# Kernel optimization log

Measured on AMD Instinct MI355X. Metric: run time of the kernel, lower is better.

The kernel has to match this reference:

```python
import jax, jax.numpy as jnp
import numpy as np

B, T, E = 2, 2048, 2048
H, D = 16, 128          # n_head, head_dim = E // H
RQ, RK, RV = 6, 2, 2    # TPA ranks


def setup_inputs() -> dict:
    key = jax.random.key(0)
    ks = jax.random.split(key, 8)
    x = jax.random.normal(ks[0], (B, T, E), jnp.float32)
    # RoPE tables: cos/sin of shape (T, 1, D//2) broadcast over (B,T,R,D//2)
    half = D // 2
    inv_freq = 1.0 / (10000.0 ** (jnp.arange(half, dtype=jnp.float32) / half))
    ang = jnp.arange(T, dtype=jnp.float32)[:, None] * inv_freq[None, :]
    cos = jnp.cos(ang)[:, None, :]
    sin = jnp.sin(ang)[:, None, :]
    s = 0.02
    W_aQ = (jax.random.normal(ks[1], (RQ * H, E), jnp.float32) * s)
    W_bQ = (jax.random.normal(ks[2], (RQ * D, E), jnp.float32) * s)
    W_aK = (jax.random.normal(ks[3], (RK * H, E), jnp.float32) * s)
    W_bK = (jax.random.normal(ks[4], (RK * D, E), jnp.float32) * s)
    W_aV = (jax.random.normal(ks[5], (RV * H, E), jnp.float32) * s)
    W_bV = (jax.random.normal(ks[6], (RV * D, E), jnp.float32) * s)
    W_cproj = (jax.random.normal(ks[7], (E, E), jnp.float32) * s)
    return {"x": x, "cos": cos, "sin": sin, "W_aQ": W_aQ, "W_bQ": W_bQ,
            "W_aK": W_aK, "W_bK": W_bK, "W_aV": W_aV, "W_bV": W_bV,
            "W_cproj": W_cproj}


def _rope(xb, cos, sin):
    # xb: (B, T, R, D); rotate-half style on split halves of D
    d = xb.shape[-1] // 2
    x1, x2 = xb[..., :d], xb[..., d:]
    return jnp.concatenate([x1 * cos + x2 * sin, -x1 * sin + x2 * cos], axis=-1)


def _rmsnorm(x):
    # F.rms_norm with no weight, default eps = finfo(dtype).eps
    eps = jnp.finfo(x.dtype).eps
    return x * jax.lax.rsqrt(jnp.mean(x * x, axis=-1, keepdims=True) + eps)


def reference(x, cos, sin, W_aQ, W_bQ, W_aK, W_bK, W_aV, W_bV, W_cproj):
    # low-rank factor projections
    a_q = (x @ W_aQ.T).reshape(B, T, RQ, H)
    a_k = (x @ W_aK.T).reshape(B, T, RK, H)
    a_v = (x @ W_aV.T).reshape(B, T, RV, H)
    b_q = (x @ W_bQ.T).reshape(B, T, RQ, D)
    b_k = (x @ W_bK.T).reshape(B, T, RK, D)
    b_v = (x @ W_bV.T).reshape(B, T, RV, D)
    # RoPE on the b factors (equivalent to RoPE on materialized Q/K)
    b_q = _rope(b_q, cos, sin)
    b_k = _rope(b_k, cos, sin)
    # tensor-product contraction: (B,T,H,D)
    q = jnp.einsum('btrh,btrd->bthd', a_q, b_q) / RQ
    k = jnp.einsum('btrh,btrd->bthd', a_k, b_k) / RK
    v = jnp.einsum('btrh,btrd->bthd', a_v, b_v) / RV
    q = _rmsnorm(q)
    k = _rmsnorm(k)
    # causal SDPA (kv_cache=None, window_size=None)
    scale = 1.0 / jnp.sqrt(jnp.asarray(D, q.dtype))
    scores = jnp.einsum('bthd,bshd->bhts', q, k) * scale
    causal = jnp.tril(jnp.ones((T, T), dtype=bool))
    scores = jnp.where(causal, scores, jnp.asarray(-jnp.inf, scores.dtype))
    p = jax.nn.softmax(scores, axis=-1)
    y = jnp.einsum('bhts,bshd->bthd', p, v).reshape(B, T, E)
    return y @ W_cproj.T
```

## Files before the change

kernel.cpp:

```cpp
#include <hip/hip_runtime.h>
#include <stdint.h>

typedef unsigned short ushort_t;
typedef __attribute__((ext_vector_type(8))) short s16x8;
typedef __attribute__((ext_vector_type(4))) float f32x4;
typedef __attribute__((ext_vector_type(16))) float f32x16;
typedef __attribute__((ext_vector_type(4))) unsigned int u32x4;

__device__ __forceinline__ unsigned short f2bf(float x) {
  union { float f; unsigned u; } a; a.f = x;
  unsigned r = a.u + 0x7fffu + ((a.u >> 16) & 1u);
  return (unsigned short)(r >> 16);
}
__device__ __forceinline__ float bf2f(unsigned short u) {
  union { unsigned u; float f; } a; a.u = ((unsigned)u) << 16;
  return a.f;
}
__device__ __forceinline__ unsigned cvtpk(float lo, float hi) {
  unsigned r;
  asm("v_cvt_pk_bf16_f32 %0, %1, %2" : "=v"(r) : "v"(lo), "v"(hi));
  return r;
}
__device__ __forceinline__ void gll16(const ushort_t* g, ushort_t* l) {
  __builtin_amdgcn_global_load_lds((const __attribute__((address_space(1))) void*)g,
                                   (__attribute__((address_space(3))) void*)l, 16, 0, 0);
}

__global__ void cvt4(const float* __restrict__ s, ushort_t* __restrict__ d, int n4) {
  int idx = blockIdx.x * blockDim.x + threadIdx.x;
  if (idx >= n4) return;
  const float4 v = *(const float4*)(s + (size_t)idx * 4);
  ushort4 o;
  o.x = f2bf(v.x); o.y = f2bf(v.y); o.z = f2bf(v.z); o.w = f2bf(v.w);
  *(ushort4*)(d + (size_t)idx * 4) = o;
}

__global__ void build_wcat(const float* __restrict__ aQ, const float* __restrict__ aK,
                           const float* __restrict__ aV, const float* __restrict__ bQ,
                           const float* __restrict__ bK, const float* __restrict__ bV,
                           ushort_t* __restrict__ W) {
  int idx = blockIdx.x * blockDim.x + threadIdx.x;
  if (idx >= 1536 * 2048) return;
  int row = idx >> 11, col = idx & 2047;
  float v = 0.f;
  if (row < 96)        v = aQ[row * 2048 + col];
  else if (row < 128)  v = aK[(row - 96) * 2048 + col];
  else if (row < 160)  v = aV[(row - 128) * 2048 + col];
  else if (row < 928)  v = bQ[(row - 160) * 2048 + col];
  else if (row < 1184) v = bK[(row - 928) * 2048 + col];
  else if (row < 1440) v = bV[(row - 1184) * 2048 + col];
  W[idx] = f2bf(v);
}

__global__ __launch_bounds__(256, 2) void gemm_bt(
    const ushort_t* __restrict__ A, const ushort_t* __restrict__ B,
    float* __restrict__ C, int M, int N, int K, int NT) {
  __shared__ ushort_t Asm[2][128 * 64];
  __shared__ ushort_t Bsm[2][128 * 64];
  const int bid = blockIdx.x;
  const int mt = bid / NT, nt = bid % NT;
  const int tid = threadIdx.x;
  const int lane = tid & 63;
  const int w = tid >> 6, wr = w >> 1, wc = w & 1;
  const int wbase = (tid & ~63);

  f32x4 acc[4][4];
#pragma unroll
  for (int a1 = 0; a1 < 4; ++a1)
#pragma unroll
    for (int b1 = 0; b1 < 4; ++b1)
#pragma unroll
      for (int e = 0; e < 4; ++e) acc[a1][b1][e] = 0.f;

  const int nkt = K >> 6;

  auto STAGE = [&](int buf, int kt) {
#pragma unroll
    for (int i = 0; i < 4; ++i) {
      int g = i * 256 + tid;
      int row = g >> 3, sc = g & 7;
      int scc = sc ^ (row & 7);
      gll16(A + (size_t)(mt * 128 + row) * K + kt * 64 + scc * 8,
            &Asm[buf][(i * 256 + wbase) * 8]);
      gll16(B + (size_t)(nt * 128 + row) * K + kt * 64 + scc * 8,
            &Bsm[buf][(i * 256 + wbase) * 8]);
    }
  };

  STAGE(0, 0);
  asm volatile("s_waitcnt vmcnt(0)" ::: "memory");
  __syncthreads();
  int cur = 0;
  for (int kt = 0; kt < nkt; ++kt) {
    if (kt + 1 < nkt) STAGE(cur ^ 1, kt + 1);
#pragma unroll
    for (int ks = 0; ks < 2; ++ks) {
      s16x8 af[4], bfv[4];
#pragma unroll
      for (int mi = 0; mi < 4; ++mi) {
        int row = wr * 64 + mi * 16 + (lane & 15);
        int colc = ks * 4 + (lane >> 4);
        af[mi] = *(const s16x8*)&Asm[cur][(row * 8 + (colc ^ (row & 7))) * 8];
      }
#pragma unroll
      for (int ni = 0; ni < 4; ++ni) {
        int row = wc * 64 + ni * 16 + (lane & 15);
        int colc = ks * 4 + (lane >> 4);
        bfv[ni] = *(const s16x8*)&Bsm[cur][(row * 8 + (colc ^ (row & 7))) * 8];
      }
#pragma unroll
      for (int mi = 0; mi < 4; ++mi)
#pragma unroll
        for (int ni = 0; ni < 4; ++ni)
          acc[mi][ni] = __builtin_amdgcn_mfma_f32_16x16x32_bf16(af[mi], bfv[ni], acc[mi][ni], 0, 0, 0);
    }
    asm volatile("s_waitcnt vmcnt(0)" ::: "memory");
    __syncthreads();
    cur ^= 1;
  }
#pragma unroll
  for (int mi = 0; mi < 4; ++mi) {
    int row0 = mt * 128 + wr * 64 + mi * 16 + ((lane >> 4) << 2);
#pragma unroll
    for (int ni = 0; ni < 4; ++ni) {
      int col = nt * 128 + wc * 64 + ni * 16 + (lane & 15);
#pragma unroll
      for (int e = 0; e < 4; ++e)
        C[(size_t)(row0 + e) * N + col] = acc[mi][ni][e];
    }
  }
}

__global__ __launch_bounds__(256) void fuse_qkv(
    const float* __restrict__ Cp, const float* __restrict__ cosT, const float* __restrict__ sinT,
    ushort_t* __restrict__ qb, ushort_t* __restrict__ kb, ushort_t* __restrict__ vb) {
  const int tok = blockIdx.x;
  const int b = tok >> 11, t = tok & 2047;
  const float* __restrict__ row = Cp + (size_t)tok * 1536;
  __shared__ float aq[96], ak[32], av[32];
  __shared__ float rbq[768], rbk[256], bvs[256];
  __shared__ float cs[64], sn[64];
  const int tid = threadIdx.x;
  if (tid < 96)        aq[tid] = row[tid];
  else if (tid < 128)  ak[tid - 96] = row[tid];
  else if (tid < 160)  av[tid - 128] = row[tid];
  else if (tid < 224) { cs[tid - 160] = cosT[t * 64 + tid - 160];
                        sn[tid - 160] = sinT[t * 64 + tid - 160]; }
  __syncthreads();
  for (int p = tid; p < 384; p += 256) {
    int r = p >> 6, d = p & 63;
    float x1 = row[160 + r * 128 + d], x2 = row[160 + r * 128 + 64 + d];
    rbq[r * 128 + d]      = x1 * cs[d] + x2 * sn[d];
    rbq[r * 128 + 64 + d] = x2 * cs[d] - x1 * sn[d];
  }
  if (tid < 128) {
    int r = tid >> 6, d = tid & 63;
    float x1 = row[928 + r * 128 + d], x2 = row[928 + r * 128 + 64 + d];
    rbk[r * 128 + d]      = x1 * cs[d] + x2 * sn[d];
    rbk[r * 128 + 64 + d] = x2 * cs[d] - x1 * sn[d];
  } else {
    int p = tid - 128;
    bvs[p] = row[1184 + p];
    bvs[p + 128] = row[1184 + 128 + p];
  }
  __syncthreads();
  const int w = tid >> 6, lane = tid & 63;
  const float QSC = 0.12751744154127828f;
#pragma unroll
  for (int j = 0; j < 4; ++j) {
    int h = w + 4 * j;
    float q0 = 0.f, q1 = 0.f;
#pragma unroll
    for (int r = 0; r < 6; ++r) {
      float a = aq[r * 16 + h];
      q0 += a * rbq[r * 128 + lane];
      q1 += a * rbq[r * 128 + 64 + lane];
    }
    q0 *= (1.f / 6.f); q1 *= (1.f / 6.f);
    float ss = q0 * q0 + q1 * q1;
#pragma unroll
    for (int o = 32; o; o >>= 1) ss += __shfl_xor(ss, o);
    float rms = rsqrtf(ss * (1.f / 128.f) + 1.1920929e-7f) * QSC;
    size_t base = ((size_t)(b * 16 + h) * 2048 + t) * 128;
    qb[base + lane]      = f2bf(q0 * rms);
    qb[base + 64 + lane] = f2bf(q1 * rms);
  }
#pragma unroll
  for (int j = 0; j < 4; ++j) {
    int h = w + 4 * j;
    float k0 = ak[h] * rbk[lane]      + ak[16 + h] * rbk[128 + lane];
    float k1 = ak[h] * rbk[64 + lane] + ak[16 + h] * rbk[192 + lane];
    k0 *= 0.5f; k1 *= 0.5f;
    float ss = k0 * k0 + k1 * k1;
#pragma unroll
    for (int o = 32; o; o >>= 1) ss += __shfl_xor(ss, o);
    float rms = rsqrtf(ss * (1.f / 128.f) + 1.1920929e-7f);
    size_t base = ((size_t)(b * 16 + h) * 2048 + t) * 128;
    kb[base + lane]      = f2bf(k0 * rms);
    kb[base + 64 + lane] = f2bf(k1 * rms);
    float v0 = 0.5f * (av[h] * bvs[lane]      + av[16 + h] * bvs[128 + lane]);
    float v1 = 0.5f * (av[h] * bvs[64 + lane] + av[16 + h] * bvs[192 + lane]);
    vb[base + lane]      = f2bf(v0);
    vb[base + 64 + lane] = f2bf(v1);
  }
}

__global__ __launch_bounds__(256) void transpose_v(const ushort_t* __restrict__ src,
                                                   ushort_t* __restrict__ dst) {
  __shared__ ushort_t sm[64 * 128];
  const int tt = blockIdx.x, bh = blockIdx.y;
  const size_t base = (size_t)bh * (2048 * 128);
  const int tid = threadIdx.x;
#pragma unroll
  for (int it = 0; it < 4; ++it) {
    int c = it * 256 + tid;
    int t = c >> 4, dc = c & 15;
    u32x4 v = *(const u32x4*)(src + base + (size_t)(tt * 64 + t) * 128 + dc * 8);
    *(u32x4*)&sm[(t * 16 + (dc ^ (t & 15))) * 8] = v;
  }
  __syncthreads();
#pragma unroll
  for (int it = 0; it < 4; ++it) {
    int c = it * 256 + tid;
    int d = c >> 3, tc = c & 7;
    ushort_t tmp[8];
#pragma unroll
    for (int jj = 0; jj < 8; ++jj) {
      int t = tc * 8 + jj;
      tmp[jj] = sm[(t * 16 + ((d >> 3) ^ (t & 15))) * 8 + (d & 7)];
    }
    *(u32x4*)(dst + base + (size_t)d * 2048 + tt * 64 + tc * 8) = *(const u32x4*)tmp;
  }
}

__global__ __launch_bounds__(256, 2) void attn(
    const ushort_t* __restrict__ Q, const ushort_t* __restrict__ Kt,
    const ushort_t* __restrict__ VT, ushort_t* __restrict__ Y,
    ushort_t* __restrict__ Ppart, float* __restrict__ Spart) {
  static const short JQT[24]  = {8,9,10,11,12,13,14,15,15,7,14,6,13,5,12,4,11,3,10,2,9,1,8,0};
  static const short JKLO[24] = {0,0,0,0,0,0,0,0,8,0,8,0,8,0,8,0,8,0,8,0,8,0,8,0};
  static const short JKHI[24] = {8,8,8,8,8,8,8,8,16,8,15,7,14,6,13,5,12,4,11,3,10,2,9,1};
  static const short JMODE[24]= {1,1,1,1,1,1,1,1,2,0,2,0,2,0,2,0,2,0,2,0,2,0,2,0};
  __shared__ ushort_t Ksm[2][64 * 128];
  __shared__ ushort_t Vsm[2][128 * 64];
  const int j = blockIdx.y, bh = blockIdx.x;
  const int qt = JQT[j];
  const int klo = (int)JKLO[j] * 128;
  const int mode = JMODE[j];
  const int kend_blk_raw = (int)JKHI[j] * 128;
  const int kend_blk = (kend_blk_raw < qt * 128 + 128) ? kend_blk_raw : qt * 128 + 128;
  const int b = bh >> 4, h = bh & 15;
  const int tid = threadIdx.x, lane = tid & 63, w = tid >> 6;
  const int hi = lane >> 5, li = lane & 31;
  const int wbase = (tid & ~63);
  const size_t hbase = (size_t)bh * (2048 * 128);
  const int wq0 = qt * 128 + w * 32;
  const int i = wq0 + li;

  s16x8 qf[8];
  const ushort_t* qrow = Q + hbase + (size_t)i * 128 + hi * 8;
#pragma unroll
  for (int c = 0; c < 8; ++c) qf[c] = *(const s16x8*)(qrow + c * 16);

  f32x16 o[4];
#pragma unroll
  for (int dt = 0; dt < 4; ++dt)
#pragma unroll
    for (int e = 0; e < 16; ++e) o[dt][e] = 0.f;
  float ssum = 0.f;

  auto STAGE = [&](int buf, int kv0s) {
#pragma unroll
    for (int it = 0; it < 4; ++it) {
      int g = it * 256 + tid;
      int row = g >> 4, sc = g & 15;
      gll16(Kt + hbase + (size_t)(kv0s + row) * 128 + (sc ^ (row & 7)) * 8,
            &Ksm[buf][(it * 256 + wbase) * 8]);
    }
#pragma unroll
    for (int it = 0; it < 4; ++it) {
      int g = it * 256 + tid;
      int d = g >> 3, sc = g & 7;
      gll16(VT + hbase + (size_t)d * 2048 + kv0s + (sc ^ (d & 7)) * 8,
            &Vsm[buf][(it * 256 + wbase) * 8]);
    }
  };

  const int nt = (kend_blk - klo) >> 6;
  STAGE(0, klo);
  asm volatile("s_waitcnt vmcnt(0)" ::: "memory");
  __syncthreads();
  int cur = 0;
  for (int t = 0; t < nt; ++t) {
    const int kv0 = klo + t * 64;
    if (t + 1 < nt) STAGE(cur ^ 1, kv0 + 64);
#pragma unroll
    for (int s = 0; s < 2; ++s) {
      const int kvs = kv0 + s * 32;
      if (kvs < wq0 + 32) {
        const int krow = s * 32 + li;
        s16x8 kf[8];
#pragma unroll
        for (int c = 0; c < 8; ++c)
          kf[c] = *(const s16x8*)&Ksm[cur][(krow * 16 + ((2 * c + hi) ^ (krow & 7))) * 8];
        f32x16 st;
#pragma unroll
        for (int e = 0; e < 16; ++e) st[e] = 0.f;
        __builtin_amdgcn_s_setprio(1);
#pragma unroll
        for (int c = 0; c < 8; ++c)
          st = __builtin_amdgcn_mfma_f32_32x32x16_bf16(kf[c], qf[c], st, 0, 0, 0);
        __builtin_amdgcn_s_setprio(0);
        float p[16]; float ls = 0.f;
        if (kvs == wq0) {
#pragma unroll
          for (int r = 0; r < 16; ++r) {
            int jrow = kvs + (r & 3) + 8 * (r >> 2) + 4 * hi;
            float pv = exp2f(st[r]);
            p[r] = (jrow > i) ? 0.f : pv;
            ls += p[r];
          }
        } else {
#pragma unroll
          for (int r = 0; r < 16; ++r) { p[r] = exp2f(st[r]); ls += p[r]; }
        }
        ls += __shfl_xor(ls, 32);
        ssum += ls;
        unsigned xp[8], xw[8];
#pragma unroll
        for (int q2 = 0; q2 < 8; ++q2) xp[q2] = cvtpk(p[2 * q2], p[2 * q2 + 1]);
#pragma unroll
        for (int q2 = 0; q2 < 8; ++q2) xw[q2] = (unsigned)__shfl_xor((int)xp[q2], 32);
        __builtin_amdgcn_s_setprio(1);
#pragma unroll
        for (int c2 = 0; c2 < 2; ++c2) {
          union { s16x8 v; unsigned u[4]; } pu;
          pu.u[0] = hi ? xw[4 * c2 + 2] : xp[4 * c2];
          pu.u[1] = hi ? xw[4 * c2 + 3] : xp[4 * c2 + 1];
          pu.u[2] = hi ? xp[4 * c2 + 2] : xw[4 * c2];
          pu.u[3] = hi ? xp[4 * c2 + 3] : xw[4 * c2 + 1];
#pragma unroll
          for (int dt = 0; dt < 4; ++dt) {
            int d = dt * 32 + li;
            s16x8 vf = *(const s16x8*)&Vsm[cur][(d * 8 + ((4 * s + 2 * c2 + hi) ^ (d & 7))) * 8];
            o[dt] = __builtin_amdgcn_mfma_f32_32x32x16_bf16(pu.v, vf, o[dt], 0, 0, 0);
          }
        }
        __builtin_amdgcn_s_setprio(0);
      }
    }
    asm volatile("s_waitcnt vmcnt(0)" ::: "memory");
    __syncthreads();
    cur ^= 1;
  }

  if (mode == 2) {
    ushort_t* Pb = Ppart + (size_t)(bh * 8 + qt - 8) * 16384;
    if (hi == 0) Spart[((size_t)bh * 16 + 8 + qt - 8) * 128 + w * 32 + li] = ssum;
#pragma unroll
    for (int r = 0; r < 16; ++r) {
      int rr = (r & 3) + 8 * (r >> 2) + 4 * hi;
#pragma unroll
      for (int dt = 0; dt < 4; ++dt)
        Pb[(size_t)(w * 32 + rr) * 128 + dt * 32 + li] = f2bf(o[dt][r]);
    }
  } else {
    if (mode == 1 && hi == 0)
      Spart[((size_t)bh * 16 + qt - 8) * 128 + w * 32 + li] = ssum;
#pragma unroll
    for (int r = 0; r < 16; ++r) {
      int rr = (r & 3) + 8 * (r >> 2) + 4 * hi;
      float rs = __shfl(ssum, rr);
      float inv = (mode == 0) ? 1.f / rs : 1.f;
      size_t yrow = (size_t)(b * 2048 + wq0 + rr);
#pragma unroll
      for (int dt = 0; dt < 4; ++dt)
        Y[yrow * 2048 + h * 128 + dt * 32 + li] = f2bf(o[dt][r] * inv);
    }
  }
}

__global__ __launch_bounds__(256) void combine(ushort_t* __restrict__ Y,
                                               const ushort_t* __restrict__ Ppart,
                                               const float* __restrict__ Spart) {
  const int qt = 8 + blockIdx.x, bh = blockIdx.y;
  const int b = bh >> 4, h = bh & 15;
  const ushort_t* Pb = Ppart + (size_t)(bh * 8 + qt - 8) * 16384;
  const float* s0 = Spart + ((size_t)bh * 16 + qt - 8) * 128;
  const float* s1 = s0 + 8 * 128;
#pragma unroll
  for (int it = 0; it < 8; ++it) {
    int c = it * 256 + threadIdx.x;
    int r = c >> 4, dc = c & 15;
    ushort_t* yp = Y + ((size_t)(b * 2048 + qt * 128 + r)) * 2048 + h * 128 + dc * 8;
    u32x4 o0 = *(const u32x4*)yp;
    u32x4 o1 = *(const u32x4*)(Pb + (size_t)r * 128 + dc * 8);
    float inv = 1.f / (s0[r] + s1[r]);
    const ushort_t* a = (const ushort_t*)&o0;
    const ushort_t* bq = (const ushort_t*)&o1;
    ushort_t res[8];
#pragma unroll
    for (int e = 0; e < 8; ++e) res[e] = f2bf((bf2f(a[e]) + bf2f(bq[e])) * inv);
    *(u32x4*)yp = *(const u32x4*)res;
  }
}

extern "C" void kernel_launch(void* const* d_in, const int* in_sizes, int n_in,
                              void* d_out, int out_size, void* d_ws, size_t ws_size,
                              hipStream_t stream) {
  const float* x    = (const float*)d_in[0];
  const float* cosT = (const float*)d_in[1];
  const float* sinT = (const float*)d_in[2];
  const float* W_aQ = (const float*)d_in[3];
  const float* W_bQ = (const float*)d_in[4];
  const float* W_aK = (const float*)d_in[5];
  const float* W_bK = (const float*)d_in[6];
  const float* W_aV = (const float*)d_in[7];
  const float* W_bV = (const float*)d_in[8];
  const float* W_c  = (const float*)d_in[9];
  float* out = (float*)d_out;

  char* ws = (char*)d_ws;
  ushort_t* xb    = (ushort_t*)(ws);
  ushort_t* Wcat  = (ushort_t*)(ws + 16777216);
  ushort_t* Wcb   = (ushort_t*)(ws + 23068672);
  float*    Cp    = (float*)   (ws + 31457280);
  ushort_t* qb    = (ushort_t*)(ws + 56623104);
  ushort_t* kb    = (ushort_t*)(ws + 73400320);
  ushort_t* vb    = (ushort_t*)(ws + 90177536);
  ushort_t* yb    = xb;
  ushort_t* vt    = (ushort_t*)(ws + 31457280);
  ushort_t* Ppart = (ushort_t*)(ws + 48234496);
  float*    Spart = (float*)   (ws + 16777216);

  cvt4<<<8192, 256, 0, stream>>>(x, xb, 2097152);
  build_wcat<<<12288, 256, 0, stream>>>(W_aQ, W_aK, W_aV, W_bQ, W_bK, W_bV, Wcat);
  cvt4<<<4096, 256, 0, stream>>>(W_c, Wcb, 1048576);

  gemm_bt<<<384, 256, 0, stream>>>(xb, Wcat, Cp, 4096, 1536, 2048, 12);
  fuse_qkv<<<4096, 256, 0, stream>>>(Cp, cosT, sinT, qb, kb, vb);
  transpose_v<<<dim3(32, 32), 256, 0, stream>>>(vb, vt);
  attn<<<dim3(32, 24), 256, 0, stream>>>(qb, kb, vt, yb, Ppart, Spart);
  combine<<<dim3(8, 32), 256, 0, stream>>>(yb, Ppart, Spart);
  gemm_bt<<<512, 256, 0, stream>>>(yb, Wcb, out, 4096, 2048, 2048, 16);
}
```

Before: 192.7 us.

## Rebalance causal attention work into 16 blocks per head with paired tasks

Reworks the attention grid from 24 to 16 blocks per head. Each block runs one or two query-tile tasks in sequence, pairing short causal tiles with split halves of long tiles so per-block work is more even. Split-K now applies only to query tiles 9-15, and the combine kernel and partial-buffer indexing are adjusted to match. It also swaps the cross-half lane exchange to permlane32_swap when that builtin is available, which cuts shuffle instructions. The cost is fewer blocks in flight and a serial second task per block.

```diff
diff --git a/kernel.cpp b/kernel.cpp
--- a/kernel.cpp
+++ b/kernel.cpp
@@ -237,37 +237,19 @@
     const ushort_t* __restrict__ Q, const ushort_t* __restrict__ Kt,
     const ushort_t* __restrict__ VT, ushort_t* __restrict__ Y,
     ushort_t* __restrict__ Ppart, float* __restrict__ Spart) {
-  static const short JQT[24]  = {8,9,10,11,12,13,14,15,15,7,14,6,13,5,12,4,11,3,10,2,9,1,8,0};
-  static const short JKLO[24] = {0,0,0,0,0,0,0,0,8,0,8,0,8,0,8,0,8,0,8,0,8,0,8,0};
-  static const short JKHI[24] = {8,8,8,8,8,8,8,8,16,8,15,7,14,6,13,5,12,4,11,3,10,2,9,1};
-  static const short JMODE[24]= {1,1,1,1,1,1,1,1,2,0,2,0,2,0,2,0,2,0,2,0,2,0,2,0};
+  static const signed char T1QT[16] = {15,15,14,14,13,13,12,12,11,11,10,10, 9, 9, 8, 7};
+  static const signed char T1LO[16] = { 0, 9, 0, 9, 0, 9, 0, 9, 0, 9, 0, 9, 0, 9, 0, 0};
+  static const signed char T1HI[16] = { 9,16, 9,15, 9,14, 9,13, 9,12, 9,11, 9,10, 9, 8};
+  static const signed char T1MD[16] = { 1, 2, 1, 2, 1, 2, 1, 2, 1, 2, 1, 2, 1, 2, 0, 0};
+  static const signed char T2QT[16] = {-1, 0,-1, 1,-1, 2,-1, 3,-1, 4,-1, 5,-1, 6,-1,-1};
   __shared__ ushort_t Ksm[2][64 * 128];
   __shared__ ushort_t Vsm[2][128 * 64];
   const int j = blockIdx.y, bh = blockIdx.x;
-  const int qt = JQT[j];
-  const int klo = (int)JKLO[j] * 128;
-  const int mode = JMODE[j];
-  const int kend_blk_raw = (int)JKHI[j] * 128;
-  const int kend_blk = (kend_blk_raw < qt * 128 + 128) ? kend_blk_raw : qt * 128 + 128;
   const int b = bh >> 4, h = bh & 15;
   const int tid = threadIdx.x, lane = tid & 63, w = tid >> 6;
   const int hi = lane >> 5, li = lane & 31;
   const int wbase = (tid & ~63);
   const size_t hbase = (size_t)bh * (2048 * 128);
-  const int wq0 = qt * 128 + w * 32;
-  const int i = wq0 + li;
-
-  s16x8 qf[8];
-  const ushort_t* qrow = Q + hbase + (size_t)i * 128 + hi * 8;
-#pragma unroll
-  for (int c = 0; c < 8; ++c) qf[c] = *(const s16x8*)(qrow + c * 16);
-
-  f32x16 o[4];
-#pragma unroll
-  for (int dt = 0; dt < 4; ++dt)
-#pragma unroll
-    for (int e = 0; e < 16; ++e) o[dt][e] = 0.f;
-  float ssum = 0.f;
 
   auto STAGE = [&](int buf, int kv0s) {
 #pragma unroll
@@ -286,96 +268,147 @@
     }
   };
 
-  const int nt = (kend_blk - klo) >> 6;
-  STAGE(0, klo);
-  asm volatile("s_waitcnt vmcnt(0)" ::: "memory");
-  __syncthreads();
-  int cur = 0;
-  for (int t = 0; t < nt; ++t) {
-    const int kv0 = klo + t * 64;
-    if (t + 1 < nt) STAGE(cur ^ 1, kv0 + 64);
-#pragma unroll
-    for (int s = 0; s < 2; ++s) {
-      const int kvs = kv0 + s * 32;
-      if (kvs < wq0 + 32) {
-        const int krow = s * 32 + li;
-        s16x8 kf[8];
-#pragma unroll
-        for (int c = 0; c < 8; ++c)
-          kf[c] = *(const s16x8*)&Ksm[cur][(krow * 16 + ((2 * c + hi) ^ (krow & 7))) * 8];
-        f32x16 st;
-#pragma unroll
-        for (int e = 0; e < 16; ++e) st[e] = 0.f;
-        __builtin_amdgcn_s_setprio(1);
-#pragma unroll
-        for (int c = 0; c < 8; ++c)
-          st = __builtin_amdgcn_mfma_f32_32x32x16_bf16(kf[c], qf[c], st, 0, 0, 0);
-        __builtin_amdgcn_s_setprio(0);
-        float p[16]; float ls = 0.f;
-        if (kvs == wq0) {
-#pragma unroll
-          for (int r = 0; r < 16; ++r) {
-            int jrow = kvs + (r & 3) + 8 * (r >> 2) + 4 * hi;
-            float pv = exp2f(st[r]);
-            p[r] = (jrow > i) ? 0.f : pv;
-            ls += p[r];
-          }
-        } else {
-#pragma unroll
-          for (int r = 0; r < 16; ++r) { p[r] = exp2f(st[r]); ls += p[r]; }
-        }
-        ls += __shfl_xor(ls, 32);
-        ssum += ls;
-        unsigned xp[8], xw[8];
-#pragma unroll
-        for (int q2 = 0; q2 < 8; ++q2) xp[q2] = cvtpk(p[2 * q2], p[2 * q2 + 1]);
-#pragma unroll
-        for (int q2 = 0; q2 < 8; ++q2) xw[q2] = (unsigned)__shfl_xor((int)xp[q2], 32);
-        __builtin_amdgcn_s_setprio(1);
-#pragma unroll
-        for (int c2 = 0; c2 < 2; ++c2) {
-          union { s16x8 v; unsigned u[4]; } pu;
-          pu.u[0] = hi ? xw[4 * c2 + 2] : xp[4 * c2];
-          pu.u[1] = hi ? xw[4 * c2 + 3] : xp[4 * c2 + 1];
-          pu.u[2] = hi ? xp[4 * c2 + 2] : xw[4 * c2];
-          pu.u[3] = hi ? xp[4 * c2 + 3] : xw[4 * c2 + 1];
-#pragma unroll
-          for (int dt = 0; dt < 4; ++dt) {
-            int d = dt * 32 + li;
-            s16x8 vf = *(const s16x8*)&Vsm[cur][(d * 8 + ((4 * s + 2 * c2 + hi) ^ (d & 7))) * 8];
-            o[dt] = __builtin_amdgcn_mfma_f32_32x32x16_bf16(pu.v, vf, o[dt], 0, 0, 0);
-          }
-        }
-        __builtin_amdgcn_s_setprio(0);
-      }
-    }
+  for (int task = 0; task < 2; ++task) {
+    int qt, klo, khi, mode;
+    if (task == 0) {
+      qt = T1QT[j]; klo = (int)T1LO[j] * 128; khi = (int)T1HI[j] * 128; mode = T1MD[j];
+    } else {
+      qt = T2QT[j]; if (qt < 0) break;
+      klo = 0; khi = (qt + 1) * 128; mode = 0;
+    }
+    const int wq0 = qt * 128 + w * 32;
+    const int i = wq0 + li;
+
+    s16x8 qf[8];
+    const ushort_t* qrow = Q + hbase + (size_t)i * 128 + hi * 8;
+#pragma unroll
+    for (int c = 0; c < 8; ++c) qf[c] = *(const s16x8*)(qrow + c * 16);
+
+    f32x16 o[4];
+#pragma unroll
+    for (int dt = 0; dt < 4; ++dt)
+#pragma unroll
+      for (int e = 0; e < 16; ++e) o[dt][e] = 0.f;
+    float ssum = 0.f;
+
+    const int nt = (khi - klo) >> 6;
+    STAGE(0, klo);
     asm volatile("s_waitcnt vmcnt(0)" ::: "memory");
     __syncthreads();
-    cur ^= 1;
-  }
-
-  if (mode == 2) {
-    ushort_t* Pb = Ppart + (size_t)(bh * 8 + qt - 8) * 16384;
-    if (hi == 0) Spart[((size_t)bh * 16 + 8 + qt - 8) * 128 + w * 32 + li] = ssum;
-#pragma unroll
-    for (int r = 0; r < 16; ++r) {
-      int rr = (r & 3) + 8 * (r >> 2) + 4 * hi;
-#pragma unroll
-      for (int dt = 0; dt < 4; ++dt)
-        Pb[(size_t)(w * 32 + rr) * 128 + dt * 32 + li] = f2bf(o[dt][r]);
-    }
-  } else {
-    if (mode == 1 && hi == 0)
-      Spart[((size_t)bh * 16 + qt - 8) * 128 + w * 32 + li] = ssum;
-#pragma unroll
-    for (int r = 0; r < 16; ++r) {
-      int rr = (r & 3) + 8 * (r >> 2) + 4 * hi;
-      float rs = __shfl(ssum, rr);
-      float inv = (mode == 0) ? 1.f / rs : 1.f;
-      size_t yrow = (size_t)(b * 2048 + wq0 + rr);
-#pragma unroll
-      for (int dt = 0; dt < 4; ++dt)
-        Y[yrow * 2048 + h * 128 + dt * 32 + li] = f2bf(o[dt][r] * inv);
+    int cur = 0;
+    for (int t = 0; t < nt; ++t) {
+      const int kv0 = klo + t * 64;
+      if (t + 1 < nt) STAGE(cur ^ 1, kv0 + 64);
+#pragma unroll
+      for (int s = 0; s < 2; ++s) {
+        const int kvs = kv0 + s * 32;
+        if (kvs < wq0 + 32) {
+          const int krow = s * 32 + li;
+          s16x8 kf[8];
+#pragma unroll
+          for (int c = 0; c < 8; ++c)
+            kf[c] = *(const s16x8*)&Ksm[cur][(krow * 16 + ((2 * c + hi) ^ (krow & 7))) * 8];
+          f32x16 st;
+#pragma unroll
+          for (int e = 0; e < 16; ++e) st[e] = 0.f;
+          __builtin_amdgcn_s_setprio(1);
+#pragma unroll
+          for (int c = 0; c < 8; ++c)
+            st = __builtin_amdgcn_mfma_f32_32x32x16_bf16(kf[c], qf[c], st, 0, 0, 0);
+          __builtin_amdgcn_s_setprio(0);
+          float p[16]; float ls = 0.f;
+          if (kvs == wq0) {
+#pragma unroll
+            for (int r = 0; r < 16; ++r) {
+              int jrow = kvs + (r & 3) + 8 * (r >> 2) + 4 * hi;
+              float pv = exp2f(st[r]);
+              p[r] = (jrow > i) ? 0.f : pv;
+              ls += p[r];
+            }
+          } else {
+#pragma unroll
+            for (int r = 0; r < 16; ++r) { p[r] = exp2f(st[r]); ls += p[r]; }
+          }
+          unsigned xp[8];
+#pragma unroll
+          for (int q2 = 0; q2 < 8; ++q2) xp[q2] = cvtpk(p[2 * q2], p[2 * q2 + 1]);
+#if __has_builtin(__builtin_amdgcn_permlane32_swap)
+          {
+            union { float f; unsigned u; } lu; lu.f = ls;
+            auto rr = __builtin_amdgcn_permlane32_swap(lu.u, lu.u, false, false);
+            union { unsigned u; float f; } r0, r1; r0.u = rr[0]; r1.u = rr[1];
+            ls = r0.f + r1.f;
+          }
+          ssum += ls;
+          __builtin_amdgcn_s_setprio(1);
+#pragma unroll
+          for (int c2 = 0; c2 < 2; ++c2) {
+            union { s16x8 v; unsigned u[4]; } pu;
+            auto r0 = __builtin_amdgcn_permlane32_swap(xp[4 * c2],     xp[4 * c2 + 2], false, false);
+            auto r1 = __builtin_amdgcn_permlane32_swap(xp[4 * c2 + 1], xp[4 * c2 + 3], false, false);
+            pu.u[0] = r0[0]; pu.u[2] = r0[1];
+            pu.u[1] = r1[0]; pu.u[3] = r1[1];
+#pragma unroll
+            for (int dt = 0; dt < 4; ++dt) {
+              int d = dt * 32 + li;
+              s16x8 vf = *(const s16x8*)&Vsm[cur][(d * 8 + ((4 * s + 2 * c2 + hi) ^ (d & 7))) * 8];
+              o[dt] = __builtin_amdgcn_mfma_f32_32x32x16_bf16(pu.v, vf, o[dt], 0, 0, 0);
+            }
+          }
+          __builtin_amdgcn_s_setprio(0);
+#else
+          ls += __shfl_xor(ls, 32);
+          ssum += ls;
+          unsigned xw[8];
+#pragma unroll
+          for (int q2 = 0; q2 < 8; ++q2) xw[q2] = (unsigned)__shfl_xor((int)xp[q2], 32);
+          __builtin_amdgcn_s_setprio(1);
+#pragma unroll
+          for (int c2 = 0; c2 < 2; ++c2) {
+            union { s16x8 v; unsigned u[4]; } pu;
+            pu.u[0] = hi ? xw[4 * c2 + 2] : xp[4 * c2];
+            pu.u[1] = hi ? xw[4 * c2 + 3] : xp[4 * c2 + 1];
+            pu.u[2] = hi ? xp[4 * c2 + 2] : xw[4 * c2];
+            pu.u[3] = hi ? xp[4 * c2 + 3] : xw[4 * c2 + 1];
+#pragma unroll
+            for (int dt = 0; dt < 4; ++dt) {
+              int d = dt * 32 + li;
+              s16x8 vf = *(const s16x8*)&Vsm[cur][(d * 8 + ((4 * s + 2 * c2 + hi) ^ (d & 7))) * 8];
+              o[dt] = __builtin_amdgcn_mfma_f32_32x32x16_bf16(pu.v, vf, o[dt], 0, 0, 0);
+            }
+          }
+          __builtin_amdgcn_s_setprio(0);
+#endif
+        }
+      }
+      asm volatile("s_waitcnt vmcnt(0)" ::: "memory");
+      __syncthreads();
+      cur ^= 1;
+    }
+
+    if (mode == 2) {
+      ushort_t* Pb = Ppart + (size_t)(bh * 7 + qt - 9) * 16384;
+      if (hi == 0) Spart[(((size_t)bh * 7 + qt - 9) * 2 + 1) * 128 + w * 32 + li] = ssum;
+#pragma unroll
+      for (int r = 0; r < 16; ++r) {
+        int rr = (r & 3) + 8 * (r >> 2) + 4 * hi;
+#pragma unroll
+        for (int dt = 0; dt < 4; ++dt)
+          Pb[(size_t)(w * 32 + rr) * 128 + dt * 32 + li] = f2bf(o[dt][r]);
+      }
+    } else {
+      if (mode == 1 && hi == 0)
+        Spart[(((size_t)bh * 7 + qt - 9) * 2 + 0) * 128 + w * 32 + li] = ssum;
+#pragma unroll
+      for (int r = 0; r < 16; ++r) {
+        int rr = (r & 3) + 8 * (r >> 2) + 4 * hi;
+        float rs = __shfl(ssum, rr);
+        float inv = (mode == 0) ? 1.f / rs : 1.f;
+        size_t yrow = (size_t)(b * 2048 + wq0 + rr);
+#pragma unroll
+        for (int dt = 0; dt < 4; ++dt)
+          Y[yrow * 2048 + h * 128 + dt * 32 + li] = f2bf(o[dt][r] * inv);
+      }
     }
   }
 }
@@ -383,16 +416,16 @@
 __global__ __launch_bounds__(256) void combine(ushort_t* __restrict__ Y,
                                                const ushort_t* __restrict__ Ppart,
                                                const float* __restrict__ Spart) {
-  const int qt = 8 + blockIdx.x, bh = blockIdx.y;
+  const int qs = blockIdx.x, bh = blockIdx.y;
   const int b = bh >> 4, h = bh & 15;
-  const ushort_t* Pb = Ppart + (size_t)(bh * 8 + qt - 8) * 16384;
-  const float* s0 = Spart + ((size_t)bh * 16 + qt - 8) * 128;
-  const float* s1 = s0 + 8 * 128;
+  const ushort_t* Pb = Ppart + (size_t)(bh * 7 + qs) * 16384;
+  const float* s0 = Spart + ((size_t)bh * 7 + qs) * 256;
+  const float* s1 = s0 + 128;
 #pragma unroll
   for (int it = 0; it < 8; ++it) {
     int c = it * 256 + threadIdx.x;
     int r = c >> 4, dc = c & 15;
-    ushort_t* yp = Y + ((size_t)(b * 2048 + qt * 128 + r)) * 2048 + h * 128 + dc * 8;
+    ushort_t* yp = Y + ((size_t)(b * 2048 + (qs + 9) * 128 + r)) * 2048 + h * 128 + dc * 8;
     u32x4 o0 = *(const u32x4*)yp;
     u32x4 o1 = *(const u32x4*)(Pb + (size_t)r * 128 + dc * 8);
     float inv = 1.f / (s0[r] + s1[r]);
@@ -440,7 +473,7 @@
   gemm_bt<<<384, 256, 0, stream>>>(xb, Wcat, Cp, 4096, 1536, 2048, 12);
   fuse_qkv<<<4096, 256, 0, stream>>>(Cp, cosT, sinT, qb, kb, vb);
   transpose_v<<<dim3(32, 32), 256, 0, stream>>>(vb, vt);
-  attn<<<dim3(32, 24), 256, 0, stream>>>(qb, kb, vt, yb, Ppart, Spart);
-  combine<<<dim3(8, 32), 256, 0, stream>>>(yb, Ppart, Spart);
+  attn<<<dim3(32, 16), 256, 0, stream>>>(qb, kb, vt, yb, Ppart, Spart);
+  combine<<<dim3(7, 32), 256, 0, stream>>>(yb, Ppart, Spart);
   gemm_bt<<<512, 256, 0, stream>>>(yb, Wcb, out, 4096, 2048, 2048, 16);
 }
```

Measured after the change: 184.0 us. -4.5%, faster.
